# Kernel tuning notes

Measured on AMD Instinct MI355X. Metric: run time of the kernel, lower is better.

Reference implementation:

```python
import jax, jax.numpy as jnp
import numpy as np
from jax import lax

B, K, STATE_DIM, ENC_DIM, H = 4096, 32, 512, 128, 128
MLP_IN = 2 * ENC_DIM + 2 * H + STATE_DIM  # 1024
H1, H2 = 1024, 512
EPS = 1e-5

PARAM_NAMES = ['w_ih_f', 'w_hh_f', 'b_ih_f', 'b_hh_f',
               'w_ih_r', 'w_hh_r', 'b_ih_r', 'b_hh_r',
               'W1', 'b1', 'g1', 'be1', 'W2', 'b2', 'g2', 'be2', 'W3', 'b3']


def setup_inputs() -> dict:
    key = jax.random.key(0)
    ks = jax.random.split(key, 24)
    s = 0.05
    d = {
        'state':  jax.random.normal(ks[0], (B, STATE_DIM), jnp.float32),
        'action': jax.random.normal(ks[1], (B, K, ENC_DIM), jnp.float32),
        # BiLSTM (torch gate order i,f,g,o), forward and reverse directions
        'w_ih_f': jax.random.normal(ks[2], (4 * H, ENC_DIM), jnp.float32) * s,
        'w_hh_f': jax.random.normal(ks[3], (4 * H, H), jnp.float32) * s,
        'b_ih_f': jax.random.normal(ks[4], (4 * H,), jnp.float32) * s,
        'b_hh_f': jax.random.normal(ks[5], (4 * H,), jnp.float32) * s,
        'w_ih_r': jax.random.normal(ks[6], (4 * H, ENC_DIM), jnp.float32) * s,
        'w_hh_r': jax.random.normal(ks[7], (4 * H, H), jnp.float32) * s,
        'b_ih_r': jax.random.normal(ks[8], (4 * H,), jnp.float32) * s,
        'b_hh_r': jax.random.normal(ks[9], (4 * H,), jnp.float32) * s,
        # QNet MLP: Linear -> BN -> ReLU (x2, dropout treated as eval/identity) -> Linear
        'W1': jax.random.normal(ks[10], (H1, MLP_IN), jnp.float32) * s,
        'b1': jnp.zeros((H1,), jnp.float32),
        'g1': jnp.ones((H1,), jnp.float32),
        'be1': jnp.zeros((H1,), jnp.float32),
        'W2': jax.random.normal(ks[11], (H2, H1), jnp.float32) * s,
        'b2': jnp.zeros((H2,), jnp.float32),
        'g2': jnp.ones((H2,), jnp.float32),
        'be2': jnp.zeros((H2,), jnp.float32),
        'W3': jax.random.normal(ks[12], (1, H2), jnp.float32) * s,
        'b3': jnp.zeros((1,), jnp.float32),
    }
    return d


def _lstm_dir(V, w_ih, w_hh, b_ih, b_hh, reverse):
    # V: (B, K, D) -> hidden states (B, K, H)
    xs = jnp.swapaxes(V, 0, 1)  # (K, B, D)
    if reverse:
        xs = xs[::-1]
    x_proj = jnp.einsum('kbd,gd->kbg', xs, w_ih) + b_ih + b_hh  # (K, B, 4H)
    h0 = jnp.zeros((V.shape[0], w_hh.shape[1]), V.dtype)

    def step(carry, xp):
        h, c = carry
        gates = xp + h @ w_hh.T
        i, f, g, o = jnp.split(gates, 4, axis=-1)
        c = jax.nn.sigmoid(f) * c + jax.nn.sigmoid(i) * jnp.tanh(g)
        h = jax.nn.sigmoid(o) * jnp.tanh(c)
        return (h, c), h

    _, hs = lax.scan(step, (h0, h0), x_proj)
    if reverse:
        hs = hs[::-1]
    return jnp.swapaxes(hs, 0, 1)  # (B, K, H)


def _bn(x, gamma, beta):
    # training-mode BatchNorm1d over flattened batch dim, per feature
    mu = jnp.mean(x, axis=0)
    var = jnp.var(x, axis=0)
    return (x - mu) * lax.rsqrt(var + EPS) * gamma + beta


def _forward(state, action, w_ih_f, w_hh_f, b_ih_f, b_hh_f,
             w_ih_r, w_hh_r, b_ih_r, b_hh_r,
             W1, b1, g1, be1, W2, b2, g2, be2, W3, b3):
    V = action  # (B, K, D)
    Of = _lstm_dir(V, w_ih_f, w_hh_f, b_ih_f, b_hh_f, reverse=False)
    Or = _lstm_dir(V, w_ih_r, w_hh_r, b_ih_r, b_hh_r, reverse=True)
    O = jnp.concatenate([Of, Or], axis=-1)  # (B, K, 2H)

    # self-attention: scores = V V^T, softmax over keys, weighted sum of V
    attn = jax.nn.softmax(jnp.einsum('bkd,bld->bkl', V, V), axis=2)  # (B, K, K)
    A = jnp.einsum('bkl,bld->bkd', attn, V)  # (B, K, D)

    S = jnp.broadcast_to(state[:, None, :], (B, K, STATE_DIM))
    X = jnp.concatenate([S, O, V, A], axis=2).reshape(B * K, MLP_IN)

    h = jax.nn.relu(_bn(X @ W1.T + b1, g1, be1))
    h = jax.nn.relu(_bn(h @ W2.T + b2, g2, be2))
    Q = (h @ W3.T + b3).reshape(B, K)
    return Q


def reference(state, action, w_ih_f, w_hh_f, b_ih_f, b_hh_f,
              w_ih_r, w_hh_r, b_ih_r, b_hh_r,
              W1, b1, g1, be1, W2, b2, g2, be2, W3, b3):
    Q = _forward(state, action, w_ih_f, w_hh_f, b_ih_f, b_hh_f,
                 w_ih_r, w_hh_r, b_ih_r, b_hh_r,
                 W1, b1, g1, be1, W2, b2, g2, be2, W3, b3)
    params = [w_ih_f, w_hh_f, b_ih_f, b_hh_f, w_ih_r, w_hh_r, b_ih_r, b_hh_r,
              W1, b1, g1, be1, W2, b2, g2, be2, W3, b3]
    reg = sum(jnp.mean(p * p) for p in params)  # L2 regularization over module params
    return Q, reg
```

## Files before the change

### kernel.cpp

```cpp
#include <hip/hip_runtime.h>
#include <cstdint>

#define NROW 131072

typedef short bf16x8 __attribute__((ext_vector_type(8)));
typedef float f32x4 __attribute__((ext_vector_type(4)));

__device__ __forceinline__ unsigned short f2bf(float f){
  unsigned u = __builtin_bit_cast(unsigned, f);
  u += 0x7fffu + ((u >> 16) & 1u);
  return (unsigned short)(u >> 16);
}
__device__ __forceinline__ float bf2f(unsigned v){
  unsigned u = v << 16; return __builtin_bit_cast(float, u);
}
__device__ __forceinline__ float sigf(float x){ return 1.0f/(1.0f + __expf(-x)); }
__device__ __forceinline__ float tanh_fast(float x){ return 2.0f/(1.0f + __expf(-2.0f*x)) - 1.0f; }

#define WS_XOA  0x00000000UL
#define WS_Y2   0x06000000UL
#define WS_SM   0x0E000000UL
#define NEED    0x0E390000UL
#define WS_YS   0x0E390000UL
#define NEED2   0x0F390000UL
#define SM_W1F  0x000000
#define SM_W2F  0x200000
#define SM_WIH  0x300000
#define SM_WHH  0x340000
#define SM_BIAS 0x380000
#define SM_STAT 0x381000
#define SM_A1   0x384000
#define SM_C1   0x385000
#define SM_A2   0x386000
#define SM_C2   0x386800

__device__ __forceinline__ void conv_frag(const float* __restrict__ src, unsigned short* __restrict__ dst,
                                          long g, long T){
  for (long i = g; i < 8192; i += T){
    int lane = (int)(i & 63);
    int blk  = (int)(i >> 6);
    int nt = blk >> 2, kt = blk & 3;
    const float* sp = src + (nt*16 + (lane&15))*128 + kt*32 + (lane>>4)*8;
    float4 a = *(const float4*)sp;
    float4 b = *(const float4*)(sp+4);
    uint4 o;
    o.x = (unsigned)f2bf(a.x) | ((unsigned)f2bf(a.y) << 16);
    o.y = (unsigned)f2bf(a.z) | ((unsigned)f2bf(a.w) << 16);
    o.z = (unsigned)f2bf(b.x) | ((unsigned)f2bf(b.y) << 16);
    o.w = (unsigned)f2bf(b.z) | ((unsigned)f2bf(b.w) << 16);
    *((uint4*)dst + i) = o;
  }
}

__global__ __launch_bounds__(256) void prep_kernel(
    const float* __restrict__ wihf, const float* __restrict__ whhf,
    const float* __restrict__ bihf, const float* __restrict__ bhhf,
    const float* __restrict__ wihr, const float* __restrict__ whhr,
    const float* __restrict__ bihr, const float* __restrict__ bhhr,
    const float* __restrict__ W1, const float* __restrict__ W2,
    unsigned short* __restrict__ W1f, unsigned short* __restrict__ W2f,
    unsigned short* __restrict__ wih, unsigned short* __restrict__ whh,
    float* __restrict__ bias){
  const long T = (long)gridDim.x * 256;
  const long g = (long)blockIdx.x * 256 + threadIdx.x;
  for (long s = g; s < 131072; s += T){
    int lane = (int)(s & 63);
    long t = s >> 6;
    int c16 = (int)(t & 7);
    long t2 = t >> 3;
    int ksub = (int)(t2 & 1);
    long t3 = t2 >> 1;
    int kb = (int)(t3 & 15);
    int chunk = (int)(t3 >> 4);
    const float* sp = W1 + (long)(chunk*128 + c16*16 + (lane&15))*1024 + kb*64 + ksub*32 + (lane>>4)*8;
    float4 a = *(const float4*)sp;
    float4 b = *(const float4*)(sp+4);
    uint4 o;
    o.x = (unsigned)f2bf(a.x) | ((unsigned)f2bf(a.y) << 16);
    o.y = (unsigned)f2bf(a.z) | ((unsigned)f2bf(a.w) << 16);
    o.z = (unsigned)f2bf(b.x) | ((unsigned)f2bf(b.y) << 16);
    o.w = (unsigned)f2bf(b.z) | ((unsigned)f2bf(b.w) << 16);
    *((uint4*)W1f + s) = o;
  }
  for (long s = g; s < 65536; s += T){
    int lane = (int)(s & 63);
    long t = s >> 6;
    int c16 = (int)(t & 31);
    long t2 = t >> 5;
    int ksub = (int)(t2 & 1);
    long t3 = t2 >> 1;
    int kh = (int)(t3 & 1);
    int nt = (int)(t3 >> 1);
    const float* sp = W2 + (long)(c16*16 + (lane&15))*1024 + nt*128 + kh*64 + ksub*32 + (lane>>4)*8;
    float4 a = *(const float4*)sp;
    float4 b = *(const float4*)(sp+4);
    uint4 o;
    o.x = (unsigned)f2bf(a.x) | ((unsigned)f2bf(a.y) << 16);
    o.y = (unsigned)f2bf(a.z) | ((unsigned)f2bf(a.w) << 16);
    o.z = (unsigned)f2bf(b.x) | ((unsigned)f2bf(b.y) << 16);
    o.w = (unsigned)f2bf(b.z) | ((unsigned)f2bf(b.w) << 16);
    *((uint4*)W2f + s) = o;
  }
  conv_frag(wihf, wih, g, T);
  conv_frag(whhf, whh, g, T);
  conv_frag(wihr, wih + 65536, g, T);
  conv_frag(whhr, whh + 65536, g, T);
  for (long i = g; i < 512; i += T){
    bias[i]       = bihf[i] + bhhf[i];
    bias[512 + i] = bihr[i] + bhhr[i];
  }
}

__global__ __launch_bounds__(256) void reg_kernel(
    const float* p0, const float* p1, const float* p2, const float* p3,
    const float* p4, const float* p5, const float* p6, const float* p7,
    const float* p8, const float* p9, const float* p10, const float* p11,
    const float* p12, const float* p13, const float* p14, const float* p15,
    const float* p16, const float* p17, float* __restrict__ out){
  const int tid = threadIdx.x;
  const long T = (long)gridDim.x * 256;
  const long g = (long)blockIdx.x * 256 + tid;
  float local = 0.f;
#define RLOOP(P, SZ) for (long i = g; i < (SZ); i += T){ float v = (P)[i]; local += v*v*(1.0f/(float)(SZ)); }
  RLOOP(p0, 65536) RLOOP(p1, 65536) RLOOP(p2, 512) RLOOP(p3, 512)
  RLOOP(p4, 65536) RLOOP(p5, 65536) RLOOP(p6, 512) RLOOP(p7, 512)
  RLOOP(p8, 1048576) RLOOP(p9, 1024) RLOOP(p10, 1024) RLOOP(p11, 1024)
  RLOOP(p12, 524288) RLOOP(p13, 512) RLOOP(p14, 512) RLOOP(p15, 512)
  RLOOP(p16, 512) RLOOP(p17, 1)
#undef RLOOP
  #pragma unroll
  for (int off=32; off>=1; off>>=1) local += __shfl_down(local, off);
  __shared__ float wsum[4];
  if ((tid & 63) == 0) wsum[tid>>6] = local;
  __syncthreads();
  if (tid == 0) atomicAdd(out, wsum[0]+wsum[1]+wsum[2]+wsum[3]);
}

__global__ __launch_bounds__(256, 1) void lstm_kernel(
    const float* __restrict__ action,
    const unsigned short* __restrict__ wih_all,
    const unsigned short* __restrict__ whh_all,
    const float* __restrict__ bias_all,
    unsigned short* __restrict__ XOA){
  const int dir = blockIdx.y;
  const int b0 = blockIdx.x * 32;
  const unsigned short* __restrict__ wih = wih_all + dir * 65536;
  const unsigned short* __restrict__ whh = whh_all + dir * 65536;
  const float* __restrict__ bias = bias_all + dir * 512;
  __shared__ __align__(16) unsigned short lh[32*136];
  const int tid = threadIdx.x;
  const int lane = tid & 63;
  const int wv = tid >> 6;
  const int l15 = lane & 15, l4 = lane >> 4;
  for (int i = tid; i < 32*136; i += 256) lh[i] = 0;
  float bias_r[2][4];
  #pragma unroll
  for (int qq=0;qq<2;qq++)
    #pragma unroll
    for (int G2=0;G2<4;G2++)
      bias_r[qq][G2] = bias[G2*128 + (2*wv+qq)*16 + l15];
  f32x4 cst[2][2];
  #pragma unroll
  for (int mt=0;mt<2;mt++)
    #pragma unroll
    for (int qq=0;qq<2;qq++){ f32x4 z = {0.f,0.f,0.f,0.f}; cst[mt][qq] = z; }
  __syncthreads();

  for (int s = 0; s < 32; s++){
    const int korig = dir ? (31 - s) : s;
    bf16x8 ha[2][4];
    #pragma unroll
    for (int mt=0;mt<2;mt++)
      #pragma unroll
      for (int kt=0;kt<4;kt++)
        ha[mt][kt] = *(const bf16x8*)&lh[(mt*16 + l15)*136 + kt*32 + l4*8];
    __syncthreads();
    bf16x8 xa[2][4];
    #pragma unroll
    for (int mt=0;mt<2;mt++)
      #pragma unroll
      for (int kt=0;kt<4;kt++){
        const float* sp = action + ((long)(b0 + mt*16 + l15)*32 + korig)*128 + kt*32 + l4*8;
        float4 a = *(const float4*)sp;
        float4 b = *(const float4*)(sp + 4);
        bf16x8 t;
        t[0]=(short)f2bf(a.x); t[1]=(short)f2bf(a.y); t[2]=(short)f2bf(a.z); t[3]=(short)f2bf(a.w);
        t[4]=(short)f2bf(b.x); t[5]=(short)f2bf(b.y); t[6]=(short)f2bf(b.z); t[7]=(short)f2bf(b.w);
        xa[mt][kt] = t;
      }
    f32x4 acc[2][2][4];
    #pragma unroll
    for (int mt=0;mt<2;mt++)
      #pragma unroll
      for (int qq=0;qq<2;qq++)
        #pragma unroll
        for (int G2=0;G2<4;G2++){
          float bb = bias_r[qq][G2];
          f32x4 z = {bb,bb,bb,bb};
          acc[mt][qq][G2] = z;
        }
    #pragma unroll
    for (int G2=0;G2<4;G2++)
      #pragma unroll
      for (int qq=0;qq<2;qq++){
        const int nt = G2*8 + 2*wv + qq;
        #pragma unroll
        for (int kt=0;kt<4;kt++){
          bf16x8 bw = *(const bf16x8*)&wih[((nt*4 + kt)*64 + lane)*8];
          acc[0][qq][G2] = __builtin_amdgcn_mfma_f32_16x16x32_bf16(xa[0][kt], bw, acc[0][qq][G2], 0,0,0);
          acc[1][qq][G2] = __builtin_amdgcn_mfma_f32_16x16x32_bf16(xa[1][kt], bw, acc[1][qq][G2], 0,0,0);
        }
        #pragma unroll
        for (int kt=0;kt<4;kt++){
          bf16x8 bw = *(const bf16x8*)&whh[((nt*4 + kt)*64 + lane)*8];
          acc[0][qq][G2] = __builtin_amdgcn_mfma_f32_16x16x32_bf16(ha[0][kt], bw, acc[0][qq][G2], 0,0,0);
          acc[1][qq][G2] = __builtin_amdgcn_mfma_f32_16x16x32_bf16(ha[1][kt], bw, acc[1][qq][G2], 0,0,0);
        }
      }
    #pragma unroll
    for (int mt=0;mt<2;mt++)
      #pragma unroll
      for (int qq=0;qq<2;qq++){
        const int hcol = (2*wv+qq)*16 + l15;
        #pragma unroll
        for (int r=0;r<4;r++){
          float iv = acc[mt][qq][0][r];
          float fv = acc[mt][qq][1][r];
          float gv = acc[mt][qq][2][r];
          float ov = acc[mt][qq][3][r];
          float c = cst[mt][qq][r];
          c = sigf(fv)*c + sigf(iv)*tanh_fast(gv);
          float h = sigf(ov)*tanh_fast(c);
          cst[mt][qq][r] = c;
          const int row = mt*16 + l4*4 + r;
          unsigned short hb = f2bf(h);
          lh[row*136 + hcol] = hb;
          XOA[((long)(b0+row)*32 + korig)*384 + dir*128 + hcol] = hb;
        }
      }
    __syncthreads();
  }
}

__global__ __launch_bounds__(256) void attn_pack(
    const float* __restrict__ action,
    unsigned short* __restrict__ XOA){
  const int b = blockIdx.x;
  const int tid = threadIdx.x;
  __shared__ __align__(16) float V[32][132];
  __shared__ __align__(16) float attw[32][33];
  const float* __restrict__ src = action + (long)b*32*128;
  for (int i = tid; i < 1024; i += 256){
    int r = i >> 5, c4 = i & 31;
    *(float4*)&V[r][c4*4] = *(const float4*)&src[r*128 + c4*4];
  }
  __syncthreads();
  const int i = tid >> 3, j0 = tid & 7;
  float sacc[4] = {0.f,0.f,0.f,0.f};
  for (int c=0;c<32;c++){
    float4 vi = *(const float4*)&V[i][c*4];
    #pragma unroll
    for (int jj=0;jj<4;jj++){
      float4 vj = *(const float4*)&V[j0 + jj*8][c*4];
      sacc[jj] += vi.x*vj.x + vi.y*vj.y + vi.z*vj.z + vi.w*vj.w;
    }
  }
  float m = fmaxf(fmaxf(sacc[0],sacc[1]), fmaxf(sacc[2],sacc[3]));
  #pragma unroll
  for (int off=1; off<8; off<<=1) m = fmaxf(m, __shfl_xor(m, off));
  float e0 = __expf(sacc[0]-m), e1 = __expf(sacc[1]-m), e2 = __expf(sacc[2]-m), e3 = __expf(sacc[3]-m);
  float ssum = e0+e1+e2+e3;
  #pragma unroll
  for (int off=1; off<8; off<<=1) ssum += __shfl_xor(ssum, off);
  float inv = 1.0f / ssum;
  attw[i][j0] = e0*inv; attw[i][j0+8] = e1*inv; attw[i][j0+16] = e2*inv; attw[i][j0+24] = e3*inv;
  __syncthreads();
  const int d0 = (tid & 7) * 16;
  float a[16];
  #pragma unroll
  for (int t=0;t<16;t++) a[t]=0.f;
  for (int j=0;j<32;j++){
    float w = attw[i][j];
    #pragma unroll
    for (int dd=0;dd<4;dd++){
      float4 v = *(const float4*)&V[j][d0 + dd*4];
      a[dd*4+0] += w*v.x; a[dd*4+1] += w*v.y; a[dd*4+2] += w*v.z; a[dd*4+3] += w*v.w;
    }
  }
  unsigned short* rowp = XOA + ((long)b*32 + i)*384;
  #pragma unroll
  for (int t=0;t<8;t++){
    ushort2 u; u.x = f2bf(a[t*2]); u.y = f2bf(a[t*2+1]);
    *(ushort2*)(rowp + 256 + d0 + t*2) = u;
  }
}

__global__ __launch_bounds__(256, 3) void ys_kernel(
    const float* __restrict__ state,
    const unsigned short* __restrict__ W1f,
    float* __restrict__ Ys){
  __shared__ __align__(16) unsigned short lA[2][8192];
  const int tid = threadIdx.x;
  const int lane = tid & 63;
  const long m0 = (long)blockIdx.x * 128;
  const int chunk = blockIdx.y;
  const int mh = (tid >> 6) >> 1, nh = (tid >> 6) & 1;
  f32x4 acc[4][4];
  #pragma unroll
  for (int a=0;a<4;a++)
    #pragma unroll
    for (int b=0;b<4;b++){ f32x4 z = {0.f,0.f,0.f,0.f}; acc[a][b] = z; }

  bf16x8 sa[4];
  const int srow = tid >> 3;
  const int sg   = (tid & 7) * 8;

  auto load_g = [&](int kb){
    const int k0 = kb << 6;
    #pragma unroll
    for (int i=0;i<4;i++){
      long r = m0 + i*32 + srow;
      const float* sp = state + r*512 + k0 + sg;
      float4 a = *(const float4*)sp;
      float4 b = *(const float4*)(sp + 4);
      bf16x8 t;
      t[0]=(short)f2bf(a.x); t[1]=(short)f2bf(a.y); t[2]=(short)f2bf(a.z); t[3]=(short)f2bf(a.w);
      t[4]=(short)f2bf(b.x); t[5]=(short)f2bf(b.y); t[6]=(short)f2bf(b.z); t[7]=(short)f2bf(b.w);
      sa[i] = t;
    }
  };
  auto write_l = [&](int buf){
    #pragma unroll
    for (int i=0;i<4;i++){
      int r = i*32 + srow;
      int j = ((tid&7) ^ (r & 7)) * 8;
      *(bf16x8*)&lA[buf][r*64 + j] = sa[i];
    }
  };
  auto compute = [&](int buf, int kb){
    #pragma unroll
    for (int ksub=0; ksub<2; ksub++){
      const unsigned short* wb = W1f + (((chunk*16 + kb)*2 + ksub)*8 + nh*4)*512 + lane*8;
      bf16x8 af[4], bg[4];
      #pragma unroll
      for (int nt=0;nt<4;nt++) bg[nt] = *(const bf16x8*)(wb + nt*512);
      #pragma unroll
      for (int mt=0;mt<4;mt++){
        int r = mh*64 + mt*16 + (lane&15);
        int p = (ksub*4 + (lane>>4)) ^ (r&7);
        af[mt] = *(const bf16x8*)&lA[buf][r*64 + p*8];
      }
      #pragma unroll
      for (int mt=0;mt<4;mt++)
        #pragma unroll
        for (int nt=0;nt<4;nt++)
          acc[mt][nt] = __builtin_amdgcn_mfma_f32_16x16x32_bf16(af[mt], bg[nt], acc[mt][nt], 0,0,0);
    }
  };

  load_g(0);
  write_l(0);
  __syncthreads();
  for (int kb = 0; kb < 8; kb++){
    if (kb + 1 < 8) load_g(kb+1);
    compute(kb & 1, kb);
    if (kb + 1 < 8) write_l((kb+1) & 1);
    __syncthreads();
  }

  #pragma unroll
  for (int nt=0; nt<4; nt++){
    int col = chunk*128 + nh*64 + nt*16 + (lane & 15);
    #pragma unroll
    for (int mt=0; mt<4; mt++){
      #pragma unroll
      for (int r=0;r<4;r++){
        long row = m0 + mh*64 + mt*16 + (lane>>4)*4 + r;
        Ys[row*1024 + col] = acc[mt][nt][r];
      }
    }
  }
}

__global__ __launch_bounds__(256, 3) void gemm1_stats(
    const float* __restrict__ state,
    const float* __restrict__ action,
    const unsigned short* __restrict__ XOA,
    const unsigned short* __restrict__ W1f,
    const float* __restrict__ Ys,
    float* __restrict__ bnsum, float* __restrict__ bnsq){
  __shared__ __align__(16) unsigned short lA[2][8192];
  const int tid = threadIdx.x;
  const int lane = tid & 63;
  const long m0 = (long)blockIdx.x * 128;
  const int chunk = blockIdx.y;
  const int mh = (tid >> 6) >> 1, nh = (tid >> 6) & 1;
  f32x4 acc[4][4];
  if (Ys){
    #pragma unroll
    for (int mt=0;mt<4;mt++){
      long rb = (m0 + mh*64 + mt*16) >> 5;
      #pragma unroll
      for (int nt=0;nt<4;nt++){
        int col = chunk*128 + nh*64 + nt*16 + (lane & 15);
        float v = Ys[rb*1024 + col];
        f32x4 z = {v,v,v,v}; acc[mt][nt] = z;
      }
    }
  } else {
    #pragma unroll
    for (int a=0;a<4;a++)
      #pragma unroll
      for (int b=0;b<4;b++){ f32x4 z = {0.f,0.f,0.f,0.f}; acc[a][b] = z; }
  }

  bf16x8 sa[4];
  const int srow = tid >> 3;
  const int sg   = (tid & 7) * 8;

  auto load_g = [&](int kb){
    const int k0 = kb << 6;
    #pragma unroll
    for (int i=0;i<4;i++){
      long r = m0 + i*32 + srow;
      bf16x8 t;
      if (k0 < 512 || (k0 >= 768 && k0 < 896)){
        const float* sp = (k0 < 512) ? (state + (r>>5)*512 + k0 + sg)
                                     : (action + r*128 + (k0-768) + sg);
        float4 a = *(const float4*)sp;
        float4 b = *(const float4*)(sp + 4);
        t[0]=(short)f2bf(a.x); t[1]=(short)f2bf(a.y); t[2]=(short)f2bf(a.z); t[3]=(short)f2bf(a.w);
        t[4]=(short)f2bf(b.x); t[5]=(short)f2bf(b.y); t[6]=(short)f2bf(b.z); t[7]=(short)f2bf(b.w);
      } else {
        int col = (k0 < 768) ? (k0 - 512) : (k0 - 640);
        t = *(const bf16x8*)&XOA[r*384 + col + sg];
      }
      sa[i] = t;
    }
  };
  auto write_l = [&](int buf){
    #pragma unroll
    for (int i=0;i<4;i++){
      int r = i*32 + srow;
      int j = ((tid&7) ^ (r & 7)) * 8;
      *(bf16x8*)&lA[buf][r*64 + j] = sa[i];
    }
  };
  auto compute = [&](int buf, int kb){
    #pragma unroll
    for (int ksub=0; ksub<2; ksub++){
      const unsigned short* wb = W1f + (((chunk*16 + kb)*2 + ksub)*8 + nh*4)*512 + lane*8;
      bf16x8 af[4], bg[4];
      #pragma unroll
      for (int nt=0;nt<4;nt++) bg[nt] = *(const bf16x8*)(wb + nt*512);
      #pragma unroll
      for (int mt=0;mt<4;mt++){
        int r = mh*64 + mt*16 + (lane&15);
        int p = (ksub*4 + (lane>>4)) ^ (r&7);
        af[mt] = *(const bf16x8*)&lA[buf][r*64 + p*8];
      }
      #pragma unroll
      for (int mt=0;mt<4;mt++)
        #pragma unroll
        for (int nt=0;nt<4;nt++)
          acc[mt][nt] = __builtin_amdgcn_mfma_f32_16x16x32_bf16(af[mt], bg[nt], acc[mt][nt], 0,0,0);
    }
  };

  const int kb_beg = Ys ? 8 : 0;
  load_g(kb_beg);
  write_l(0);
  __syncthreads();
  for (int kb = kb_beg; kb < 16; kb++){
    if (kb + 1 < 16) load_g(kb+1);
    compute(kb & 1, kb);
    if (kb + 1 < 16) write_l((kb+1) & 1);
    __syncthreads();
  }

  #pragma unroll
  for (int nt=0; nt<4; nt++){
    int col = chunk*128 + nh*64 + nt*16 + (lane & 15);
    float s = 0.f, q = 0.f;
    #pragma unroll
    for (int mt=0; mt<4; mt++)
      #pragma unroll
      for (int r=0;r<4;r++){
        float v = acc[mt][nt][r];
        s += v; q += v*v;
      }
    s += __shfl_down(s, 32); q += __shfl_down(q, 32);
    s += __shfl_down(s, 16); q += __shfl_down(q, 16);
    if (lane < 16){
      atomicAdd(&bnsum[col], s);
      atomicAdd(&bnsq[col], q);
    }
  }
}

__global__ void bn_finalize(const float* __restrict__ sum, const float* __restrict__ sq,
                            const float* __restrict__ gamma, const float* __restrict__ beta,
                            float* __restrict__ a, float* __restrict__ c, int N){
  int i = blockIdx.x*256 + threadIdx.x;
  if (i >= N) return;
  const float invM = 1.0f / 131072.0f;
  float mu = sum[i]*invM;
  float var = sq[i]*invM - mu*mu;
  float s = rsqrtf(var + 1e-5f) * gamma[i];
  a[i] = s;
  c[i] = beta[i] - mu*s;
}

__global__ __launch_bounds__(256, 2) void gemm12(
    const float* __restrict__ state,
    const float* __restrict__ action,
    const unsigned short* __restrict__ XOA,
    const unsigned short* __restrict__ W1f,
    const unsigned short* __restrict__ W2f,
    const float* __restrict__ Ys,
    const float* __restrict__ a1, const float* __restrict__ c1,
    unsigned short* __restrict__ Y2,
    float* __restrict__ bnsum, float* __restrict__ bnsq){
  __shared__ __align__(16) unsigned short stage[2][8192];
  __shared__ __align__(16) unsigned short h1c[64*136];
  const int tid = threadIdx.x;
  const int lane = tid & 63;
  const int w = tid >> 6;
  const long m0 = (long)blockIdx.x * 64;
  const int rowgA = w >> 1, colgA = w & 1;
  const int rgB = w >> 1, cgB = w & 1;

  f32x4 acc2[2][16];
  #pragma unroll
  for (int a=0;a<2;a++)
    #pragma unroll
    for (int b=0;b<16;b++){ f32x4 z = {0.f,0.f,0.f,0.f}; acc2[a][b] = z; }

  bf16x8 xs[4];
  const int kbp_beg = Ys ? 4 : 0;

  for (int nt = 0; nt < 8; nt++){
    f32x4 acc1[2][4];
    if (Ys){
      #pragma unroll
      for (int rt=0;rt<2;rt++){
        long rb = (m0 + rowgA*32 + rt*16) >> 5;
        #pragma unroll
        for (int ct=0;ct<4;ct++){
          int col = nt*128 + colgA*64 + ct*16 + (lane & 15);
          float v = Ys[rb*1024 + col];
          f32x4 z = {v,v,v,v}; acc1[rt][ct] = z;
        }
      }
    } else {
      #pragma unroll
      for (int a=0;a<2;a++)
        #pragma unroll
        for (int b=0;b<4;b++){ f32x4 z = {0.f,0.f,0.f,0.f}; acc1[a][b] = z; }
    }

    auto load_gA = [&](int kbp){
      const int k0 = kbp << 7;
      #pragma unroll
      for (int i=0;i<4;i++){
        int ch = i*256 + tid;
        int row = ch >> 4, kc = ch & 15;
        long R = m0 + row;
        bf16x8 t;
        if (kbp < 4 || kbp == 6){
          const float* sp = (kbp < 4) ? (state + (R>>5)*512 + k0 + kc*8)
                                      : (action + R*128 + (k0-768) + kc*8);
          float4 a = *(const float4*)sp;
          float4 b = *(const float4*)(sp + 4);
          t[0]=(short)f2bf(a.x); t[1]=(short)f2bf(a.y); t[2]=(short)f2bf(a.z); t[3]=(short)f2bf(a.w);
          t[4]=(short)f2bf(b.x); t[5]=(short)f2bf(b.y); t[6]=(short)f2bf(b.z); t[7]=(short)f2bf(b.w);
        } else {
          int col = (kbp < 6) ? (k0 - 512) : (k0 - 640);
          t = *(const bf16x8*)&XOA[R*384 + col + kc*8];
        }
        xs[i] = t;
      }
    };
    auto write_lA = [&](int buf){
      #pragma unroll
      for (int i=0;i<4;i++){
        int ch = i*256 + tid;
        int row = ch >> 4, kc = ch & 15;
        int j = (kc ^ (row & 7)) * 8;
        *(bf16x8*)&stage[buf][row*128 + j] = xs[i];
      }
    };
    auto computeA = [&](int buf, int kbp){
      #pragma unroll
      for (int ks4=0; ks4<4; ks4++){
        const int kb = kbp*2 + (ks4 >> 1);
        const int ksub = ks4 & 1;
        const unsigned short* wb = W1f + (((nt*16 + kb)*2 + ksub)*8 + colgA*4)*512 + lane*8;
        bf16x8 af[2], bg[4];
        #pragma unroll
        for (int ct=0;ct<4;ct++) bg[ct] = *(const bf16x8*)(wb + ct*512);
        #pragma unroll
        for (int rt=0;rt<2;rt++){
          int r = rowgA*32 + rt*16 + (lane&15);
          int p = (ks4*4 + (lane>>4)) ^ (r&7);
          af[rt] = *(const bf16x8*)&stage[buf][r*128 + p*8];
        }
        #pragma unroll
        for (int rt=0;rt<2;rt++)
          #pragma unroll
          for (int ct=0;ct<4;ct++)
            acc1[rt][ct] = __builtin_amdgcn_mfma_f32_16x16x32_bf16(af[rt], bg[ct], acc1[rt][ct], 0,0,0);
      }
    };

    load_gA(kbp_beg); write_lA(0); __syncthreads();
    for (int kbp = kbp_beg; kbp < 8; kbp++){
      if (kbp + 1 < 8) load_gA(kbp+1);
      computeA(kbp & 1, kbp);
      if (kbp + 1 < 8) write_lA((kbp+1) & 1);
      __syncthreads();
    }

    #pragma unroll
    for (int ct=0;ct<4;ct++){
      int lcol = colgA*64 + ct*16 + (lane&15);
      float av = a1[nt*128 + lcol];
      float cv = c1[nt*128 + lcol];
      #pragma unroll
      for (int rt=0;rt<2;rt++)
        #pragma unroll
        for (int r=0;r<4;r++){
          int row = rowgA*32 + rt*16 + (lane>>4)*4 + r;
          float h = fmaxf(fmaf(acc1[rt][ct][r], av, cv), 0.f);
          h1c[row*136 + lcol] = f2bf(h);
        }
    }
    __syncthreads();

    #pragma unroll
    for (int kh=0;kh<2;kh++){
      #pragma unroll
      for (int ksub=0;ksub<2;ksub++){
        bf16x8 af[2];
        #pragma unroll
        for (int rt=0;rt<2;rt++){
          int row = rgB*32 + rt*16 + (lane&15);
          af[rt] = *(const bf16x8*)&h1c[row*136 + kh*64 + ksub*32 + (lane>>4)*8];
        }
        #pragma unroll
        for (int cth=0;cth<2;cth++){
          const unsigned short* wb = W2f + ((((nt*2 + kh)*2 + ksub)*32) + cgB*16 + cth*8)*512 + lane*8;
          bf16x8 bg[8];
          #pragma unroll
          for (int ct=0;ct<8;ct++) bg[ct] = *(const bf16x8*)(wb + ct*512);
          #pragma unroll
          for (int rt=0;rt<2;rt++)
            #pragma unroll
            for (int ct=0;ct<8;ct++)
              acc2[rt][cth*8+ct] = __builtin_amdgcn_mfma_f32_16x16x32_bf16(af[rt], bg[ct], acc2[rt][cth*8+ct], 0,0,0);
        }
      }
    }
  }

  #pragma unroll
  for (int ct=0;ct<16;ct++){
    int col = cgB*256 + ct*16 + (lane&15);
    float s = 0.f, q = 0.f;
    #pragma unroll
    for (int rt=0;rt<2;rt++)
      #pragma unroll
      for (int r=0;r<4;r++){
        long row = m0 + rgB*32 + rt*16 + (lane>>4)*4 + r;
        unsigned short ub = f2bf(acc2[rt][ct][r]);
        Y2[row*512 + col] = ub;
        float vq = bf2f(ub);
        s += vq; q += vq*vq;
      }
    s += __shfl_down(s, 32); q += __shfl_down(q, 32);
    s += __shfl_down(s, 16); q += __shfl_down(q, 16);
    if (lane < 16){
      atomicAdd(&bnsum[col], s);
      atomicAdd(&bnsq[col], q);
    }
  }
}

__global__ __launch_bounds__(256) void final_kernel(
    const unsigned short* __restrict__ Y2,
    const float* __restrict__ a2, const float* __restrict__ c2,
    const float* __restrict__ W3, const float* __restrict__ b3, float* __restrict__ Q){
  const int tid = threadIdx.x;
  const int lane = tid & 63, wv = tid >> 6;
  const int wid = blockIdx.x*4 + wv;
  const int cb = lane*8;
  float4 a0 = *(const float4*)&a2[cb], a1 = *(const float4*)&a2[cb+4];
  float4 c0 = *(const float4*)&c2[cb], c1 = *(const float4*)&c2[cb+4];
  float4 w0 = *(const float4*)&W3[cb], w1 = *(const float4*)&W3[cb+4];
  const float b3v = b3[0];
  for (long row = wid; row < NROW; row += 4096){
    uint4 u = *(const uint4*)(Y2 + row*512 + cb);
    float y0 = bf2f(u.x & 0xffffu), y1 = bf2f(u.x >> 16);
    float y2 = bf2f(u.y & 0xffffu), y3 = bf2f(u.y >> 16);
    float y4 = bf2f(u.z & 0xffffu), y5 = bf2f(u.z >> 16);
    float y6 = bf2f(u.w & 0xffffu), y7 = bf2f(u.w >> 16);
    float t = fmaxf(fmaf(y0,a0.x,c0.x),0.f)*w0.x
            + fmaxf(fmaf(y1,a0.y,c0.y),0.f)*w0.y
            + fmaxf(fmaf(y2,a0.z,c0.z),0.f)*w0.z
            + fmaxf(fmaf(y3,a0.w,c0.w),0.f)*w0.w
            + fmaxf(fmaf(y4,a1.x,c1.x),0.f)*w1.x
            + fmaxf(fmaf(y5,a1.y,c1.y),0.f)*w1.y
            + fmaxf(fmaf(y6,a1.z,c1.z),0.f)*w1.z
            + fmaxf(fmaf(y7,a1.w,c1.w),0.f)*w1.w;
    #pragma unroll
    for (int off=32; off>=1; off>>=1) t += __shfl_down(t, off);
    if (lane == 0) Q[row] = t + b3v;
  }
}

extern "C" void kernel_launch(void* const* d_in, const int* in_sizes, int n_in,
                              void* d_out, int out_size, void* d_ws, size_t ws_size,
                              hipStream_t stream){
  (void)in_sizes; (void)n_in; (void)out_size;
  if (ws_size < NEED) return;
  const bool use_ys = (ws_size >= NEED2);

  const float* state  = (const float*)d_in[0];
  const float* action = (const float*)d_in[1];
  const float* w_ih_f = (const float*)d_in[2];
  const float* w_hh_f = (const float*)d_in[3];
  const float* b_ih_f = (const float*)d_in[4];
  const float* b_hh_f = (const float*)d_in[5];
  const float* w_ih_r = (const float*)d_in[6];
  const float* w_hh_r = (const float*)d_in[7];
  const float* b_ih_r = (const float*)d_in[8];
  const float* b_hh_r = (const float*)d_in[9];
  const float* W1  = (const float*)d_in[10];
  const float* b1  = (const float*)d_in[11];
  const float* g1  = (const float*)d_in[12];
  const float* be1 = (const float*)d_in[13];
  const float* W2  = (const float*)d_in[14];
  const float* b2  = (const float*)d_in[15];
  const float* g2  = (const float*)d_in[16];
  const float* be2 = (const float*)d_in[17];
  const float* W3  = (const float*)d_in[18];
  const float* b3  = (const float*)d_in[19];
  (void)b1; (void)b2;

  char* ws = (char*)d_ws;
  unsigned short* XOA = (unsigned short*)(ws + WS_XOA);
  unsigned short* Y2  = (unsigned short*)(ws + WS_Y2);
  float* Ysp = use_ys ? (float*)(ws + WS_YS) : nullptr;
  char* sm = ws + WS_SM;
  unsigned short* W1f = (unsigned short*)(sm + SM_W1F);
  unsigned short* W2f = (unsigned short*)(sm + SM_W2F);
  unsigned short* wih = (unsigned short*)(sm + SM_WIH);
  unsigned short* whh = (unsigned short*)(sm + SM_WHH);
  float* bias   = (float*)(sm + SM_BIAS);
  float* bnsum1 = (float*)(sm + SM_STAT);
  float* bnsq1  = (float*)(sm + SM_STAT + 0x1000);
  float* bnsum2 = (float*)(sm + SM_STAT + 0x2000);
  float* bnsq2  = (float*)(sm + SM_STAT + 0x2800);
  float* a1 = (float*)(sm + SM_A1);
  float* c1 = (float*)(sm + SM_C1);
  float* a2 = (float*)(sm + SM_A2);
  float* c2 = (float*)(sm + SM_C2);
  float* qout = (float*)d_out;
  float* regout = qout + 131072;

  hipMemsetAsync(bnsum1, 0, 0x3000, stream);
  hipMemsetAsync(regout, 0, 4, stream);

  prep_kernel<<<1024, 256, 0, stream>>>(w_ih_f, w_hh_f, b_ih_f, b_hh_f,
                                        w_ih_r, w_hh_r, b_ih_r, b_hh_r,
                                        W1, W2, W1f, W2f, wih, whh, bias);
  reg_kernel<<<256, 256, 0, stream>>>(w_ih_f, w_hh_f, b_ih_f, b_hh_f,
                                      w_ih_r, w_hh_r, b_ih_r, b_hh_r,
                                      W1, b1, g1, be1, W2, b2, g2, be2, W3, b3, regout);
  if (use_ys)
    ys_kernel<<<dim3(32, 8), 256, 0, stream>>>(state, W1f, Ysp);
  lstm_kernel<<<dim3(128,2), 256, 0, stream>>>(action, wih, whh, bias, XOA);
  attn_pack<<<4096, 256, 0, stream>>>(action, XOA);
  gemm1_stats<<<dim3(1024,8), 256, 0, stream>>>(state, action, XOA, W1f, Ysp, bnsum1, bnsq1);
  bn_finalize<<<4, 256, 0, stream>>>(bnsum1, bnsq1, g1, be1, a1, c1, 1024);
  gemm12<<<2048, 256, 0, stream>>>(state, action, XOA, W1f, W2f, Ysp, a1, c1, Y2, bnsum2, bnsq2);
  bn_finalize<<<2, 256, 0, stream>>>(bnsum2, bnsq2, g2, be2, a2, c2, 512);
  final_kernel<<<1024, 256, 0, stream>>>(Y2, a2, c2, W3, b3, qout);
}
```

Baseline: 1.406 ms.

## Stage full per-row input tile in LDS once and reuse across all output chunks

gemm1_stats and gemm12 now load the 64-row x 512-wide non-state input slice (LSTM output, action, attention) into LDS once per block. It is reused across all eight 128-column output chunks instead of being re-streamed per chunk through a double buffer. gemm1_stats is regridded from 1024x8 blocks of 128 rows to 2048 blocks of 64 rows that loop over chunks, the h1c buffer gets an XOR swizzle instead of padding, and the no-Ys fallback path is removed. This cuts repeated global reads and conversions of X, at the cost of 64KB of LDS per block (lower occupancy) and no load/compute overlap.

New measurement: 1.225 ms. 1.15x faster.

```diff
diff --git a/kernel.cpp b/kernel.cpp
--- a/kernel.cpp
+++ b/kernel.cpp
@@ -20,7 +20,6 @@
 #define WS_XOA  0x00000000UL
 #define WS_Y2   0x06000000UL
 #define WS_SM   0x0E000000UL
-#define NEED    0x0E390000UL
 #define WS_YS   0x0E390000UL
 #define NEED2   0x0F390000UL
 #define SM_W1F  0x000000
@@ -382,118 +381,96 @@
   }
 }
 
-__global__ __launch_bounds__(256, 3) void gemm1_stats(
-    const float* __restrict__ state,
+__global__ __launch_bounds__(256, 2) void gemm1_stats(
     const float* __restrict__ action,
     const unsigned short* __restrict__ XOA,
     const unsigned short* __restrict__ W1f,
     const float* __restrict__ Ys,
     float* __restrict__ bnsum, float* __restrict__ bnsq){
-  __shared__ __align__(16) unsigned short lA[2][8192];
+  __shared__ __align__(16) unsigned short stage[4][8192];
   const int tid = threadIdx.x;
   const int lane = tid & 63;
-  const long m0 = (long)blockIdx.x * 128;
-  const int chunk = blockIdx.y;
-  const int mh = (tid >> 6) >> 1, nh = (tid >> 6) & 1;
-  f32x4 acc[4][4];
-  if (Ys){
-    #pragma unroll
-    for (int mt=0;mt<4;mt++){
-      long rb = (m0 + mh*64 + mt*16) >> 5;
-      #pragma unroll
-      for (int nt=0;nt<4;nt++){
-        int col = chunk*128 + nh*64 + nt*16 + (lane & 15);
-        float v = Ys[rb*1024 + col];
-        f32x4 z = {v,v,v,v}; acc[mt][nt] = z;
-      }
-    }
-  } else {
-    #pragma unroll
-    for (int a=0;a<4;a++)
-      #pragma unroll
-      for (int b=0;b<4;b++){ f32x4 z = {0.f,0.f,0.f,0.f}; acc[a][b] = z; }
-  }
-
-  bf16x8 sa[4];
-  const int srow = tid >> 3;
-  const int sg   = (tid & 7) * 8;
-
-  auto load_g = [&](int kb){
-    const int k0 = kb << 6;
+  const int w = tid >> 6;
+  const long m0 = (long)blockIdx.x * 64;
+  const int rowg = w >> 1, colg = w & 1;
+
+  #pragma unroll
+  for (int kbp = 4; kbp < 8; kbp++){
     #pragma unroll
     for (int i=0;i<4;i++){
-      long r = m0 + i*32 + srow;
+      int ch = i*256 + tid;
+      int row = ch >> 4, kc = ch & 15;
+      long R = m0 + row;
       bf16x8 t;
-      if (k0 < 512 || (k0 >= 768 && k0 < 896)){
-        const float* sp = (k0 < 512) ? (state + (r>>5)*512 + k0 + sg)
-                                     : (action + r*128 + (k0-768) + sg);
+      if (kbp == 6){
+        const float* sp = action + R*128 + kc*8;
         float4 a = *(const float4*)sp;
         float4 b = *(const float4*)(sp + 4);
         t[0]=(short)f2bf(a.x); t[1]=(short)f2bf(a.y); t[2]=(short)f2bf(a.z); t[3]=(short)f2bf(a.w);
         t[4]=(short)f2bf(b.x); t[5]=(short)f2bf(b.y); t[6]=(short)f2bf(b.z); t[7]=(short)f2bf(b.w);
       } else {
-        int col = (k0 < 768) ? (k0 - 512) : (k0 - 640);
-        t = *(const bf16x8*)&XOA[r*384 + col + sg];
-      }
-      sa[i] = t;
-    }
-  };
-  auto write_l = [&](int buf){
-    #pragma unroll
-    for (int i=0;i<4;i++){
-      int r = i*32 + srow;
-      int j = ((tid&7) ^ (r & 7)) * 8;
-      *(bf16x8*)&lA[buf][r*64 + j] = sa[i];
-    }
-  };
-  auto compute = [&](int buf, int kb){
-    #pragma unroll
-    for (int ksub=0; ksub<2; ksub++){
-      const unsigned short* wb = W1f + (((chunk*16 + kb)*2 + ksub)*8 + nh*4)*512 + lane*8;
-      bf16x8 af[4], bg[4];
-      #pragma unroll
-      for (int nt=0;nt<4;nt++) bg[nt] = *(const bf16x8*)(wb + nt*512);
-      #pragma unroll
-      for (int mt=0;mt<4;mt++){
-        int r = mh*64 + mt*16 + (lane&15);
-        int p = (ksub*4 + (lane>>4)) ^ (r&7);
-        af[mt] = *(const bf16x8*)&lA[buf][r*64 + p*8];
-      }
-      #pragma unroll
-      for (int mt=0;mt<4;mt++)
-        #pragma unroll
-        for (int nt=0;nt<4;nt++)
-          acc[mt][nt] = __builtin_amdgcn_mfma_f32_16x16x32_bf16(af[mt], bg[nt], acc[mt][nt], 0,0,0);
-    }
-  };
-
-  const int kb_beg = Ys ? 8 : 0;
-  load_g(kb_beg);
-  write_l(0);
+        int col = (kbp < 6) ? ((kbp-4)*128) : 256;
+        t = *(const bf16x8*)&XOA[R*384 + col + kc*8];
+      }
+      int j = (kc ^ (row & 7)) * 8;
+      *(bf16x8*)&stage[kbp-4][row*128 + j] = t;
+    }
+  }
   __syncthreads();
-  for (int kb = kb_beg; kb < 16; kb++){
-    if (kb + 1 < 16) load_g(kb+1);
-    compute(kb & 1, kb);
-    if (kb + 1 < 16) write_l((kb+1) & 1);
-    __syncthreads();
-  }
-
-  #pragma unroll
-  for (int nt=0; nt<4; nt++){
-    int col = chunk*128 + nh*64 + nt*16 + (lane & 15);
-    float s = 0.f, q = 0.f;
-    #pragma unroll
-    for (int mt=0; mt<4; mt++)
-      #pragma unroll
-      for (int r=0;r<4;r++){
-        float v = acc[mt][nt][r];
-        s += v; q += v*v;
-      }
-    s += __shfl_down(s, 32); q += __shfl_down(q, 32);
-    s += __shfl_down(s, 16); q += __shfl_down(q, 16);
-    if (lane < 16){
-      atomicAdd(&bnsum[col], s);
-      atomicAdd(&bnsq[col], q);
+
+  const long rbb = m0 >> 5;
+  for (int chunk = 0; chunk < 8; chunk++){
+    f32x4 acc[2][4];
+    #pragma unroll
+    for (int rt=0;rt<2;rt++){
+      long rb = rbb + ((rowg*32 + rt*16) >> 5);
+      #pragma unroll
+      for (int ct=0;ct<4;ct++){
+        int col = chunk*128 + colg*64 + ct*16 + (lane & 15);
+        float v = Ys[rb*1024 + col];
+        f32x4 z = {v,v,v,v}; acc[rt][ct] = z;
+      }
+    }
+    #pragma unroll
+    for (int kbp=4; kbp<8; kbp++){
+      #pragma unroll
+      for (int ks4=0; ks4<4; ks4++){
+        const int kb = kbp*2 + (ks4 >> 1);
+        const int ksub = ks4 & 1;
+        const unsigned short* wb = W1f + (((chunk*16 + kb)*2 + ksub)*8 + colg*4)*512 + lane*8;
+        bf16x8 af[2], bg[4];
+        #pragma unroll
+        for (int ct=0;ct<4;ct++) bg[ct] = *(const bf16x8*)(wb + ct*512);
+        #pragma unroll
+        for (int rt=0;rt<2;rt++){
+          int r = rowg*32 + rt*16 + (lane&15);
+          int p = (ks4*4 + (lane>>4)) ^ (r&7);
+          af[rt] = *(const bf16x8*)&stage[kbp-4][r*128 + p*8];
+        }
+        #pragma unroll
+        for (int rt=0;rt<2;rt++)
+          #pragma unroll
+          for (int ct=0;ct<4;ct++)
+            acc[rt][ct] = __builtin_amdgcn_mfma_f32_16x16x32_bf16(af[rt], bg[ct], acc[rt][ct], 0,0,0);
+      }
+    }
+    #pragma unroll
+    for (int ct=0;ct<4;ct++){
+      int col = chunk*128 + colg*64 + ct*16 + (lane & 15);
+      float s = 0.f, q = 0.f;
+      #pragma unroll
+      for (int rt=0;rt<2;rt++)
+        #pragma unroll
+        for (int r=0;r<4;r++){
+          float v = acc[rt][ct][r];
+          s += v; q += v*v;
+        }
+      s += __shfl_down(s, 32); q += __shfl_down(q, 32);
+      s += __shfl_down(s, 16); q += __shfl_down(q, 16);
+      if (lane < 16){
+        atomicAdd(&bnsum[col], s);
+        atomicAdd(&bnsq[col], q);
+      }
     }
   }
 }
@@ -512,7 +489,6 @@
 }
 
 __global__ __launch_bounds__(256, 2) void gemm12(
-    const float* __restrict__ state,
     const float* __restrict__ action,
     const unsigned short* __restrict__ XOA,
     const unsigned short* __restrict__ W1f,
@@ -521,8 +497,8 @@
     const float* __restrict__ a1, const float* __restrict__ c1,
     unsigned short* __restrict__ Y2,
     float* __restrict__ bnsum, float* __restrict__ bnsq){
-  __shared__ __align__(16) unsigned short stage[2][8192];
-  __shared__ __align__(16) unsigned short h1c[64*136];
+  __shared__ __align__(16) unsigned short stage[4][8192];
+  __shared__ __align__(16) unsigned short h1c[8192];
   const int tid = threadIdx.x;
   const int lane = tid & 63;
   const int w = tid >> 6;
@@ -530,67 +506,52 @@
   const int rowgA = w >> 1, colgA = w & 1;
   const int rgB = w >> 1, cgB = w & 1;
 
+  #pragma unroll
+  for (int kbp = 4; kbp < 8; kbp++){
+    #pragma unroll
+    for (int i=0;i<4;i++){
+      int ch = i*256 + tid;
+      int row = ch >> 4, kc = ch & 15;
+      long R = m0 + row;
+      bf16x8 t;
+      if (kbp == 6){
+        const float* sp = action + R*128 + kc*8;
+        float4 a = *(const float4*)sp;
+        float4 b = *(const float4*)(sp + 4);
+        t[0]=(short)f2bf(a.x); t[1]=(short)f2bf(a.y); t[2]=(short)f2bf(a.z); t[3]=(short)f2bf(a.w);
+        t[4]=(short)f2bf(b.x); t[5]=(short)f2bf(b.y); t[6]=(short)f2bf(b.z); t[7]=(short)f2bf(b.w);
+      } else {
+        int col = (kbp < 6) ? ((kbp-4)*128) : 256;
+        t = *(const bf16x8*)&XOA[R*384 + col + kc*8];
+      }
+      int j = (kc ^ (row & 7)) * 8;
+      *(bf16x8*)&stage[kbp-4][row*128 + j] = t;
+    }
+  }
+
   f32x4 acc2[2][16];
   #pragma unroll
   for (int a=0;a<2;a++)
     #pragma unroll
     for (int b=0;b<16;b++){ f32x4 z = {0.f,0.f,0.f,0.f}; acc2[a][b] = z; }
 
-  bf16x8 xs[4];
-  const int kbp_beg = Ys ? 4 : 0;
+  const long rbb = m0 >> 5;
+  __syncthreads();
 
   for (int nt = 0; nt < 8; nt++){
     f32x4 acc1[2][4];
-    if (Ys){
-      #pragma unroll
-      for (int rt=0;rt<2;rt++){
-        long rb = (m0 + rowgA*32 + rt*16) >> 5;
-        #pragma unroll
-        for (int ct=0;ct<4;ct++){
-          int col = nt*128 + colgA*64 + ct*16 + (lane & 15);
-          float v = Ys[rb*1024 + col];
-          f32x4 z = {v,v,v,v}; acc1[rt][ct] = z;
-        }
-      }
-    } else {
-      #pragma unroll
-      for (int a=0;a<2;a++)
-        #pragma unroll
-        for (int b=0;b<4;b++){ f32x4 z = {0.f,0.f,0.f,0.f}; acc1[a][b] = z; }
-    }
-
-    auto load_gA = [&](int kbp){
-      const int k0 = kbp << 7;
-      #pragma unroll
-      for (int i=0;i<4;i++){
-        int ch = i*256 + tid;
-        int row = ch >> 4, kc = ch & 15;
-        long R = m0 + row;
-        bf16x8 t;
-        if (kbp < 4 || kbp == 6){
-          const float* sp = (kbp < 4) ? (state + (R>>5)*512 + k0 + kc*8)
-                                      : (action + R*128 + (k0-768) + kc*8);
-          float4 a = *(const float4*)sp;
-          float4 b = *(const float4*)(sp + 4);
-          t[0]=(short)f2bf(a.x); t[1]=(short)f2bf(a.y); t[2]=(short)f2bf(a.z); t[3]=(short)f2bf(a.w);
-          t[4]=(short)f2bf(b.x); t[5]=(short)f2bf(b.y); t[6]=(short)f2bf(b.z); t[7]=(short)f2bf(b.w);
-        } else {
-          int col = (kbp < 6) ? (k0 - 512) : (k0 - 640);
-          t = *(const bf16x8*)&XOA[R*384 + col + kc*8];
-        }
-        xs[i] = t;
-      }
-    };
-    auto write_lA = [&](int buf){
-      #pragma unroll
-      for (int i=0;i<4;i++){
-        int ch = i*256 + tid;
-        int row = ch >> 4, kc = ch & 15;
-        int j = (kc ^ (row & 7)) * 8;
-        *(bf16x8*)&stage[buf][row*128 + j] = xs[i];
-      }
-    };
-    auto computeA = [&](int buf, int kbp){
+    #pragma unroll
+    for (int rt=0;rt<2;rt++){
+      long rb = rbb + ((rowgA*32 + rt*16) >> 5);
+      #pragma unroll
+      for (int ct=0;ct<4;ct++){
+        int col = nt*128 + colgA*64 + ct*16 + (lane & 15);
+        float v = Ys[rb*1024 + col];
+        f32x4 z = {v,v,v,v}; acc1[rt][ct] = z;
+      }
+    }
+    #pragma unroll
+    for (int kbp=4; kbp<8; kbp++){
       #pragma unroll
       for (int ks4=0; ks4<4; ks4++){
         const int kb = kbp*2 + (ks4 >> 1);
@@ -603,7 +564,7 @@
         for (int rt=0;rt<2;rt++){
           int r = rowgA*32 + rt*16 + (lane&15);
           int p = (ks4*4 + (lane>>4)) ^ (r&7);
-          af[rt] = *(const bf16x8*)&stage[buf][r*128 + p*8];
+          af[rt] = *(const bf16x8*)&stage[kbp-4][r*128 + p*8];
         }
         #pragma unroll
         for (int rt=0;rt<2;rt++)
@@ -611,15 +572,9 @@
           for (int ct=0;ct<4;ct++)
             acc1[rt][ct] = __builtin_amdgcn_mfma_f32_16x16x32_bf16(af[rt], bg[ct], acc1[rt][ct], 0,0,0);
       }
-    };
-
-    load_gA(kbp_beg); write_lA(0); __syncthreads();
-    for (int kbp = kbp_beg; kbp < 8; kbp++){
-      if (kbp + 1 < 8) load_gA(kbp+1);
-      computeA(kbp & 1, kbp);
-      if (kbp + 1 < 8) write_lA((kbp+1) & 1);
-      __syncthreads();
-    }
+    }
+
+    __syncthreads();
 
     #pragma unroll
     for (int ct=0;ct<4;ct++){
@@ -632,7 +587,8 @@
         for (int r=0;r<4;r++){
           int row = rowgA*32 + rt*16 + (lane>>4)*4 + r;
           float h = fmaxf(fmaf(acc1[rt][ct][r], av, cv), 0.f);
-          h1c[row*136 + lcol] = f2bf(h);
+          int sc = (lcol & 7) | ((((lcol >> 3) ^ (row & 7)) & 15) << 3);
+          h1c[row*128 + sc] = f2bf(h);
         }
     }
     __syncthreads();
@@ -645,7 +601,9 @@
         #pragma unroll
         for (int rt=0;rt<2;rt++){
           int row = rgB*32 + rt*16 + (lane&15);
-          af[rt] = *(const bf16x8*)&h1c[row*136 + kh*64 + ksub*32 + (lane>>4)*8];
+          int g0 = kh*8 + ksub*4 + (lane>>4);
+          int gs = g0 ^ (row & 7);
+          af[rt] = *(const bf16x8*)&h1c[row*128 + gs*8];
         }
         #pragma unroll
         for (int cth=0;cth<2;cth++){
@@ -722,8 +680,7 @@
                               void* d_out, int out_size, void* d_ws, size_t ws_size,
                               hipStream_t stream){
   (void)in_sizes; (void)n_in; (void)out_size;
-  if (ws_size < NEED) return;
-  const bool use_ys = (ws_size >= NEED2);
+  if (ws_size < NEED2) return;
 
   const float* state  = (const float*)d_in[0];
   const float* action = (const float*)d_in[1];
@@ -750,7 +707,7 @@
   char* ws = (char*)d_ws;
   unsigned short* XOA = (unsigned short*)(ws + WS_XOA);
   unsigned short* Y2  = (unsigned short*)(ws + WS_Y2);
-  float* Ysp = use_ys ? (float*)(ws + WS_YS) : nullptr;
+  float* Ysp = (float*)(ws + WS_YS);
   char* sm = ws + WS_SM;
   unsigned short* W1f = (unsigned short*)(sm + SM_W1F);
   unsigned short* W2f = (unsigned short*)(sm + SM_W2F);
@@ -777,13 +734,12 @@
   reg_kernel<<<256, 256, 0, stream>>>(w_ih_f, w_hh_f, b_ih_f, b_hh_f,
                                       w_ih_r, w_hh_r, b_ih_r, b_hh_r,
                                       W1, b1, g1, be1, W2, b2, g2, be2, W3, b3, regout);
-  if (use_ys)
-    ys_kernel<<<dim3(32, 8), 256, 0, stream>>>(state, W1f, Ysp);
+  ys_kernel<<<dim3(32, 8), 256, 0, stream>>>(state, W1f, Ysp);
   lstm_kernel<<<dim3(128,2), 256, 0, stream>>>(action, wih, whh, bias, XOA);
   attn_pack<<<4096, 256, 0, stream>>>(action, XOA);
-  gemm1_stats<<<dim3(1024,8), 256, 0, stream>>>(state, action, XOA, W1f, Ysp, bnsum1, bnsq1);
+  gemm1_stats<<<2048, 256, 0, stream>>>(action, XOA, W1f, Ysp, bnsum1, bnsq1);
   bn_finalize<<<4, 256, 0, stream>>>(bnsum1, bnsq1, g1, be1, a1, c1, 1024);
-  gemm12<<<2048, 256, 0, stream>>>(state, action, XOA, W1f, W2f, Ysp, a1, c1, Y2, bnsum2, bnsq2);
+  gemm12<<<2048, 256, 0, stream>>>(action, XOA, W1f, W2f, Ysp, a1, c1, Y2, bnsum2, bnsq2);
   bn_finalize<<<2, 256, 0, stream>>>(bnsum2, bnsq2, g2, be2, a2, c2, 512);
   final_kernel<<<1024, 256, 0, stream>>>(Y2, a2, c2, W3, b3, qout);
 }
```
